# Kernel optimization log

Hardware: AMD Instinct MI355X
Metric: run time of the kernel (lower is better)

The kernel has to match this reference:

```python
import jax, jax.numpy as jnp
import numpy as np

SR = 8                      # search_range
MO = 2 * SR + 1             # max_offset = 17
NC = MO * MO                # 289 cost-volume channels


def _l2_normalize(x, eps=1e-12):
    # torch F.normalize(p=2, dim=1): x / max(||x||_2, eps)
    n = jnp.sqrt(jnp.sum(x * x, axis=1, keepdims=True))
    return x / jnp.maximum(n, eps)


def _conv2d(x, w, b, pad, groups=1):
    out = jax.lax.conv_general_dilated(
        x, w, window_strides=(1, 1), padding=[(pad, pad), (pad, pad)],
        feature_group_count=groups,
        dimension_numbers=('NCHW', 'OIHW', 'NCHW'))
    return out + b[None, :, None, None]


def _cost_volume(x1, x2, sr, norm_both=False):
    x1 = _l2_normalize(x1)
    if norm_both:
        x2 = _l2_normalize(x2)
    bs, c, h, w = x1.shape
    padded = jnp.pad(x2, ((0, 0), (0, 0), (sr, sr), (sr, sr)))
    mo = 2 * sr + 1
    # offsets in (j outer, i inner) order, matching the original double loop
    jj, ii = jnp.meshgrid(jnp.arange(mo), jnp.arange(mo), indexing='ij')
    offs = jnp.stack([jj.reshape(-1), ii.reshape(-1)], axis=-1)  # [mo^2, 2]

    def step(carry, off):
        sl = jax.lax.dynamic_slice(padded, (0, 0, off[0], off[1]), (bs, c, h, w))
        return carry, jnp.mean(x1 * sl, axis=1)  # [bs, h, w]

    _, cv = jax.lax.scan(step, None, offs)       # [mo^2, bs, h, w]
    cv = jnp.transpose(cv, (1, 0, 2, 3))          # [bs, mo^2, h, w]
    return jax.nn.leaky_relu(cv, 0.1)


def setup_inputs() -> dict:
    key = jax.random.key(0)
    ks = jax.random.split(key, 8)
    bs, c, h, w = 4, 256, 64, 64
    scale = 0.05
    return {
        'f1': jax.random.normal(ks[0], (bs, c, h, w), jnp.float32),
        'f2': jax.random.normal(ks[1], (bs, c, h, w), jnp.float32),
        'att_w': jax.random.normal(ks[2], (NC, 1, 7, 7), jnp.float32) * scale,
        'att_b': jax.random.normal(ks[3], (NC,), jnp.float32) * scale,
        'agg1_w': jax.random.normal(ks[4], (NC // 2, NC, 3, 3), jnp.float32) * scale,
        'agg1_b': jax.random.normal(ks[5], (NC // 2,), jnp.float32) * scale,
        'agg2_w': jax.random.normal(ks[6], (49, NC // 2, 3, 3), jnp.float32) * scale,
        'agg2_b': jax.random.normal(ks[7], (49,), jnp.float32) * scale,
    }


def reference(f1, f2, att_w, att_b, agg1_w, agg1_b, agg2_w, agg2_b):
    match_vol = _cost_volume(f1, f2, SR, norm_both=False)          # [bs,289,h,w]
    att = _conv2d(match_vol, att_w, att_b, pad=3, groups=NC)       # depthwise 7x7
    att_vol = match_vol * att
    h1 = jax.nn.relu(_conv2d(att_vol, agg1_w, agg1_b, pad=1))      # Conv(289->144,3)
    out = jax.nn.relu(_conv2d(h1, agg2_w, agg2_b, pad=1))          # Conv(144->49,3)
    return out
```

## Files before the change

### kernel.cpp

```cpp
#include <hip/hip_runtime.h>
#include <hip/hip_bf16.h>

#define BS   4
#define C    256
#define HW   4096
#define NPIX 16384
#define NCH  289
#define MO   17
#define PH   80
#define PW   80
#define C1   144
#define C2   49
#define ASTR 264
#define ICP  320
#define IC3  192
#define CVP  70
#define CVC  320
#define CH64 72

typedef __bf16  bf16x8 __attribute__((ext_vector_type(8)));
typedef float   f32x4  __attribute__((ext_vector_type(4)));
typedef unsigned short us8 __attribute__((ext_vector_type(8)));

__global__ void fused_norm_transpose(const float* __restrict__ f1,
                                     unsigned short* __restrict__ dst) {
    __shared__ float tileT[32 * 257];
    __shared__ float invS[32];
    int blk = blockIdx.x;
    int pblk = blk & 127, b = blk >> 7;
    int p0 = pblk * 32;
    int t = threadIdx.x;
    int tx = t & 31, ty = t >> 5;
    const float* s = f1 + (size_t)b * C * HW;
#pragma unroll
    for (int i = 0; i < 32; ++i) {
        int c = ty + 8 * i;
        tileT[tx * 257 + c] = s[(size_t)c * HW + p0 + tx];
    }
    __syncthreads();
    int lane = t & 63, wave = t >> 6;
    int px = wave * 8 + (lane >> 3);
    int l = lane & 7;
    float ssum = 0.f;
#pragma unroll
    for (int j = 0; j < 32; ++j) {
        float v = tileT[px * 257 + l + 8 * j];
        ssum += v * v;
    }
    ssum += __shfl_xor(ssum, 1);
    ssum += __shfl_xor(ssum, 2);
    ssum += __shfl_xor(ssum, 4);
    if (l == 0) invS[px] = 1.0f / fmaxf(sqrtf(ssum), 1e-12f);
    __syncthreads();
#pragma unroll 4
    for (int p = 0; p < 32; ++p) {
        float v = tileT[p * 257 + t] * invS[p];
        __hip_bfloat16 hb = __float2bfloat16(v);
        dst[((size_t)b * HW + p0 + p) * C + t] = *(unsigned short*)&hb;
    }
}

__global__ void transpose_pad_kernel(const float* __restrict__ src,
                                     unsigned short* __restrict__ dst) {
    __shared__ float tile[32][33];
    int blk = blockIdx.x;
    int pblk = blk & 127;
    int cblk = (blk >> 7) & 7;
    int b    = blk >> 10;
    int tx = threadIdx.x & 31, ty = threadIdx.x >> 5;
    int c0 = cblk * 32, p0 = pblk * 32;
    const float* s = src + (size_t)b * C * HW;
#pragma unroll
    for (int i = 0; i < 4; ++i) {
        int c = c0 + ty + 8 * i;
        tile[ty + 8 * i][tx] = s[(size_t)c * HW + p0 + tx];
    }
    __syncthreads();
#pragma unroll
    for (int i = 0; i < 4; ++i) {
        int p = p0 + ty + 8 * i;
        float v = tile[tx][ty + 8 * i];
        int c = c0 + tx;
        int h = p >> 6, w = p & 63;
        __hip_bfloat16 hb = __float2bfloat16(v);
        dst[(((size_t)b * PH + h + 8) * PW + (w + 8)) * C + c] = *(unsigned short*)&hb;
    }
}

__device__ __forceinline__ void halo_zero_dev(unsigned short* p, int H, int halo,
                                              int Cc, int blk, int t) {
    int W = H;
    int inter = H - 2 * halo;
    int total_pos = H * W - inter * inter;
    int chunks = Cc >> 3;
    size_t tot = (size_t)total_pos * chunks * BS;
    size_t idx = (size_t)blk * 256 + t;
    if (idx >= tot) return;
    int c8 = (int)(idx % chunks);
    size_t r = idx / chunks;
    int pos = (int)(r % total_pos);
    int b = (int)(r / total_pos);
    int h, w;
    int topbot = 2 * halo * W;
    if (pos < halo * W) { h = pos / W; w = pos % W; }
    else if (pos < topbot) { int q = pos - halo * W; h = H - halo + q / W; w = q % W; }
    else {
        int q = pos - topbot;
        int row = q / (2 * halo), off = q % (2 * halo);
        h = halo + row;
        w = (off < halo) ? off : (W - 2 * halo + off);
    }
    us8 z = {0, 0, 0, 0, 0, 0, 0, 0};
    *(us8*)&p[(((size_t)b * H + h) * W + w) * Cc + c8 * 8] = z;
}

__global__ void prep_kernel(unsigned short* __restrict__ x2bf, unsigned short* __restrict__ cvp,
                            unsigned short* __restrict__ avp, unsigned short* __restrict__ h1p,
                            const float* __restrict__ w1, unsigned short* __restrict__ wb1,
                            const float* __restrict__ w2, unsigned short* __restrict__ wb2,
                            const float* __restrict__ att_w, float* __restrict__ wdwp) {
    int blk = blockIdx.x;
    int t = threadIdx.x;
    if (blk < 1152) { halo_zero_dev(x2bf, PH, 8, C, blk, t); return; }
    if (blk < 1655) { halo_zero_dev(cvp, CVP, 3, CVC, blk - 1152, t); return; }
    if (blk < 1818) { halo_zero_dev(avp, 66, 1, ICP, blk - 1655, t); return; }
    if (blk < 1916) { halo_zero_dev(h1p, 66, 1, IC3, blk - 1818, t); return; }
    if (blk < 3536) {
        int idx = (blk - 1916) * 256 + t;
        int tap = idx / (C1 * ICP);
        int r = idx - tap * (C1 * ICP);
        int oc = r / ICP;
        int ic = r - oc * ICP;
        float v = (ic < NCH) ? w1[((size_t)(oc * NCH + ic)) * 9 + tap] : 0.f;
        __hip_bfloat16 hb = __float2bfloat16(v);
        wb1[idx] = *(unsigned short*)&hb;
        return;
    }
    if (blk < 3968) {
        int idx = (blk - 3536) * 256 + t;
        int tap = idx / (64 * IC3);
        int r = idx - tap * (64 * IC3);
        int oc = r / IC3;
        int ic = r - oc * IC3;
        float v = (oc < C2 && ic < C1) ? w2[((size_t)(oc * C1 + ic)) * 9 + tap] : 0.f;
        __hip_bfloat16 hb = __float2bfloat16(v);
        wb2[idx] = *(unsigned short*)&hb;
        return;
    }
    {
        int idx = (blk - 3968) * 256 + t;
        if (idx >= 49 * CVC) return;
        int tap = idx / CVC;
        int ch = idx - tap * CVC;
        wdwp[idx] = (ch < NCH) ? att_w[ch * 49 + tap] : 0.f;
    }
}

__global__ void cv_mfma_kernel(const unsigned short* __restrict__ x1b,
                               const unsigned short* __restrict__ x2b,
                               unsigned short* __restrict__ cvp) {
    __shared__ __align__(16) unsigned short x2s[2][32 * ASTR];
    int i = blockIdx.x;
    int xcd = i & 7;
    int j = i >> 3;
    int hq = xcd * 2 + (j & 1);
    int jj = j >> 1;
    int wseg = jj & 3;
    int b = jj >> 2;
    int h0 = hq * 4;
    int w0 = wseg * 16;
    int t = threadIdx.x;
    int wave = t >> 6, lane = t & 63;
    int lrow = lane & 15, quad = lane >> 4;
    int h = h0 + wave;

    const unsigned short* x1p = x1b + ((size_t)b * HW + h * 64 + w0) * C;
    bf16x8 a[8];
#pragma unroll
    for (int kk = 0; kk < 8; ++kk)
        a[kk] = *(const bf16x8*)&x1p[(size_t)lrow * C + kk * 32 + quad * 8];

    const unsigned short* x2base = x2b + (size_t)b * PH * PW * C;

    {
        const unsigned short* rowp = x2base + ((size_t)h0 * PW + w0) * C;
#pragma unroll
        for (int s = 0; s < 4; ++s) {
            int v = t + s * 256;
            int col = v >> 5, ch8 = v & 31;
            *(us8*)&x2s[0][col * ASTR + ch8 * 8] = *(const us8*)&rowp[(size_t)col * C + ch8 * 8];
        }
    }
    __syncthreads();

    for (int rr = 0; rr < 20; ++rr) {
        us8 pr[4];
        bool dop = (rr + 1 < 20);
        if (dop) {
            const unsigned short* rowp = x2base + ((size_t)(h0 + rr + 1) * PW + w0) * C;
#pragma unroll
            for (int s = 0; s < 4; ++s) {
                int v = t + s * 256;
                int col = v >> 5, ch8 = v & 31;
                pr[s] = *(const us8*)&rowp[(size_t)col * C + ch8 * 8];
            }
        }

        int dj = rr - wave;
        if ((unsigned)dj <= 16u) {
            const unsigned short* xs = x2s[rr & 1];
#pragma unroll
            for (int c = 0; c < 2; ++c) {
                f32x4 acc = {0.f, 0.f, 0.f, 0.f};
#pragma unroll
                for (int kk = 0; kk < 8; ++kk) {
                    bf16x8 bb = *(const bf16x8*)&xs[(c * 16 + lrow) * ASTR + kk * 32 + quad * 8];
                    acc = __builtin_amdgcn_mfma_f32_16x16x32_bf16(a[kk], bb, acc, 0, 0, 0);
                }
#pragma unroll
                for (int r = 0; r < 4; ++r) {
                    int px_l = quad * 4 + r;
                    int di = c * 16 + lrow - px_l;
                    if ((unsigned)di <= 16u) {
                        float v = acc[r] * (1.0f / 256.0f);
                        v = (v > 0.f) ? v : 0.1f * v;
                        __hip_bfloat16 hb = __float2bfloat16(v);
                        cvp[(((size_t)b * CVP + h + 3) * CVP + (w0 + px_l + 3)) * CVC + dj * MO + di] =
                            *(unsigned short*)&hb;
                    }
                }
            }
        }

        if (dop) {
            unsigned short* dst = x2s[(rr + 1) & 1];
#pragma unroll
            for (int s = 0; s < 4; ++s) {
                int v = t + s * 256;
                int col = v >> 5, ch8 = v & 31;
                *(us8*)&dst[col * ASTR + ch8 * 8] = pr[s];
            }
            __syncthreads();
        }
    }
}

__global__ void dw_att_tiled(const unsigned short* __restrict__ cvp,
                             const float* __restrict__ wdwp,
                             const float* __restrict__ att_b, unsigned short* __restrict__ av_pad) {
    __shared__ float actS[14 * 14 * 64];
    __shared__ float wdwS[49 * 64];
    int i = blockIdx.x;
    int ty = i & 7;
    int j = i >> 3;
    int cc = j % 5;
    int rest = j / 5;
    int tx = rest & 7, b = rest >> 3;
    int x0 = tx * 8, y0 = ty * 8;
    int c0 = cc * 64;
    int t = threadIdx.x;

    const unsigned short* cvb = cvp + (((size_t)b * CVP + y0) * CVP + x0) * CVC + c0;
    for (int v = t; v < 14 * 14 * 8; v += 256) {
        int rc = v >> 3, c8v = v & 7;
        int yy = rc / 14, xx = rc - yy * 14;
        bf16x8 raw = *(const bf16x8*)&cvb[((size_t)yy * CVP + xx) * CVC + c8v * 8];
        f32x4 lo, hi;
#pragma unroll
        for (int e = 0; e < 4; ++e) { lo[e] = (float)raw[e]; hi[e] = (float)raw[e + 4]; }
        *(f32x4*)&actS[rc * 64 + c8v * 8] = lo;
        *(f32x4*)&actS[rc * 64 + c8v * 8 + 4] = hi;
    }
    for (int v = t; v < 49 * 64; v += 256) {
        int tap = v >> 6, ch = v & 63;
        wdwS[v] = wdwp[tap * CVC + c0 + ch];
    }
    __syncthreads();

    int ch_l = t & 63, pgrp = t >> 6;
    int ch = c0 + ch_l;
    float bv = (ch < NCH) ? att_b[ch] : 0.f;
    float acc[16];
#pragma unroll
    for (int ii = 0; ii < 16; ++ii) acc[ii] = bv;

    for (int dy = 0; dy < 7; ++dy) {
#pragma unroll
        for (int dx = 0; dx < 7; ++dx) {
            float wv = wdwS[(dy * 7 + dx) * 64 + ch_l];
#pragma unroll
            for (int ii = 0; ii < 16; ++ii) {
                int py = pgrp * 2 + (ii >> 3), px = ii & 7;
                float a = actS[((py + dy) * 14 + (px + dx)) * 64 + ch_l];
                acc[ii] += a * wv;
            }
        }
    }

    if (ch < NCH) {
#pragma unroll
        for (int ii = 0; ii < 16; ++ii) {
            int py = pgrp * 2 + (ii >> 3), px = ii & 7;
            float c0v = actS[((py + 3) * 14 + (px + 3)) * 64 + ch_l];
            __hip_bfloat16 hb = __float2bfloat16(c0v * acc[ii]);
            av_pad[(((size_t)b * 66 + y0 + py + 1) * 66 + (x0 + px + 1)) * ICP + ch] =
                *(unsigned short*)&hb;
        }
    }
}

__global__ void agg1_mfma_kernel(const unsigned short* __restrict__ av_pad,
                                 const unsigned short* __restrict__ wb1,
                                 const float* __restrict__ bias,
                                 unsigned short* __restrict__ h1p) {
    __shared__ __align__(16) unsigned short aS2[2][66 * CH64];
    __shared__ __align__(16) unsigned short bS[2][C1 * CH64];
    int i = blockIdx.x;
    int xcd = i & 7;
    int j = i >> 3;
    int h = xcd * 8 + (j & 7);
    int b = j >> 3;
    int t = threadIdx.x;
    int wave = t >> 6, lane = t & 63;
    int lrow = lane & 15, quad = lane >> 4;
    int ot0 = (wave == 0) ? 0 : (wave * 2 + 1);
    int nt  = (wave == 0) ? 3 : 2;

    f32x4 acc[4][3];
#pragma unroll
    for (int m = 0; m < 4; ++m)
#pragma unroll
        for (int ii = 0; ii < 3; ++ii) acc[m][ii] = (f32x4){0.f, 0.f, 0.f, 0.f};

    const unsigned short* avb = av_pad + (((size_t)b * 66 + h) * 66) * ICP;

    {
        const unsigned short* arow = avb;
#pragma unroll
        for (int s = 0; s < 2; ++s) {
            int v = t + s * 256;
            *(us8*)&aS2[0][(v >> 3) * CH64 + (v & 7) * 8] =
                *(const us8*)&arow[(size_t)(v >> 3) * ICP + (v & 7) * 8];
        }
        if (t < 16) {
            int v = t + 512;
            *(us8*)&aS2[0][(v >> 3) * CH64 + (v & 7) * 8] =
                *(const us8*)&arow[(size_t)(v >> 3) * ICP + (v & 7) * 8];
        }
#pragma unroll
        for (int s = 0; s < 4; ++s) {
            int v = t + s * 256;
            *(us8*)&bS[0][(v >> 3) * CH64 + (v & 7) * 8] =
                *(const us8*)&wb1[(size_t)(v >> 3) * ICP + (v & 7) * 8];
        }
        if (t < 128) {
            int v = t + 1024;
            *(us8*)&bS[0][(v >> 3) * CH64 + (v & 7) * 8] =
                *(const us8*)&wb1[(size_t)(v >> 3) * ICP + (v & 7) * 8];
        }
    }
    __syncthreads();

    for (int k = 0; k < 45; ++k) {
        int rr = k % 15;
        int dx = rr % 3;
        int abuf = (k / 3) & 1, bbuf = k & 1;

        us8 br[5], ar[3];
        int kn = k + 1;
        bool do_b = (kn < 45);
        bool do_a = do_b && (kn % 3 == 0);
        int dyn = kn / 15, rn = kn % 15;
        int ccin = rn / 3, dxn = rn % 3;
        if (do_b) {
            const unsigned short* wt = wb1 + ((size_t)(dyn * 3 + dxn) * C1) * ICP + ccin * 64;
#pragma unroll
            for (int s = 0; s < 4; ++s) {
                int v = t + s * 256;
                br[s] = *(const us8*)&wt[(size_t)(v >> 3) * ICP + (v & 7) * 8];
            }
            if (t < 128) {
                int v = t + 1024;
                br[4] = *(const us8*)&wt[(size_t)(v >> 3) * ICP + (v & 7) * 8];
            }
        }
        if (do_a) {
            const unsigned short* arow = avb + (size_t)dyn * 66 * ICP + ccin * 64;
#pragma unroll
            for (int s = 0; s < 2; ++s) {
                int v = t + s * 256;
                ar[s] = *(const us8*)&arow[(size_t)(v >> 3) * ICP + (v & 7) * 8];
            }
            if (t < 16) {
                int v = t + 512;
                ar[2] = *(const us8*)&arow[(size_t)(v >> 3) * ICP + (v & 7) * 8];
            }
        }

        const unsigned short* aP = aS2[abuf];
        const unsigned short* bP = bS[bbuf];
#pragma unroll
        for (int cc2 = 0; cc2 < 2; ++cc2) {
            bf16x8 bfr[3];
#pragma unroll
            for (int ii = 0; ii < 3; ++ii)
                if (ii < nt)
                    bfr[ii] = *(const bf16x8*)&bP[((ot0 + ii) * 16 + lrow) * CH64 + cc2 * 32 + quad * 8];
#pragma unroll
            for (int m = 0; m < 4; ++m) {
                bf16x8 af = *(const bf16x8*)&aP[(m * 16 + lrow + dx) * CH64 + cc2 * 32 + quad * 8];
#pragma unroll
                for (int ii = 0; ii < 3; ++ii)
                    if (ii < nt)
                        acc[m][ii] = __builtin_amdgcn_mfma_f32_16x16x32_bf16(af, bfr[ii], acc[m][ii], 0, 0, 0);
            }
        }

        if (do_b) {
            unsigned short* dst = bS[bbuf ^ 1];
#pragma unroll
            for (int s = 0; s < 4; ++s) {
                int v = t + s * 256;
                *(us8*)&dst[(v >> 3) * CH64 + (v & 7) * 8] = br[s];
            }
            if (t < 128) {
                int v = t + 1024;
                *(us8*)&dst[(v >> 3) * CH64 + (v & 7) * 8] = br[4];
            }
        }
        if (do_a) {
            unsigned short* dst = aS2[abuf ^ 1];
#pragma unroll
            for (int s = 0; s < 2; ++s) {
                int v = t + s * 256;
                *(us8*)&dst[(v >> 3) * CH64 + (v & 7) * 8] = ar[s];
            }
            if (t < 16) {
                int v = t + 512;
                *(us8*)&dst[(v >> 3) * CH64 + (v & 7) * 8] = ar[2];
            }
        }
        if (do_b) __syncthreads();
    }

    size_t rowbase = ((size_t)b * 66 + h + 1) * 66;
#pragma unroll
    for (int m = 0; m < 4; ++m)
#pragma unroll
        for (int ii = 0; ii < 3; ++ii)
            if (ii < nt) {
                int oc = (ot0 + ii) * 16 + lrow;
                float bv = bias[oc];
#pragma unroll
                for (int r = 0; r < 4; ++r) {
                    int w = m * 16 + quad * 4 + r;
                    float val = fmaxf(acc[m][ii][r] + bv, 0.f);
                    __hip_bfloat16 hb = __float2bfloat16(val);
                    h1p[(rowbase + (w + 1)) * IC3 + oc] = *(unsigned short*)&hb;
                }
            }
}

__global__ void agg2_mfma_kernel(const unsigned short* __restrict__ h1p,
                                 const unsigned short* __restrict__ wb2,
                                 const float* __restrict__ bias, float* __restrict__ out) {
    __shared__ __align__(16) unsigned short aS2[2][66 * CH64];
    __shared__ __align__(16) unsigned short bS2[2][64 * CH64];
    int i = blockIdx.x;
    int xcd = i & 7;
    int j = i >> 3;
    int h = xcd * 8 + (j & 7);
    int b = j >> 3;
    int t = threadIdx.x;
    int wave = t >> 6, lane = t & 63;
    int lrow = lane & 15, quad = lane >> 4;
    int pt = wave;

    f32x4 acc[4];
#pragma unroll
    for (int ot = 0; ot < 4; ++ot) acc[ot] = (f32x4){0.f, 0.f, 0.f, 0.f};

    const unsigned short* h1b = h1p + (((size_t)b * 66 + h) * 66) * IC3;

    {
#pragma unroll
        for (int s = 0; s < 2; ++s) {
            int v = t + s * 256;
            *(us8*)&aS2[0][(v >> 3) * CH64 + (v & 7) * 8] =
                *(const us8*)&h1b[(size_t)(v >> 3) * IC3 + (v & 7) * 8];
        }
        if (t < 16) {
            int v = t + 512;
            *(us8*)&aS2[0][(v >> 3) * CH64 + (v & 7) * 8] =
                *(const us8*)&h1b[(size_t)(v >> 3) * IC3 + (v & 7) * 8];
        }
#pragma unroll
        for (int s = 0; s < 2; ++s) {
            int v = t + s * 256;
            *(us8*)&bS2[0][(v >> 3) * CH64 + (v & 7) * 8] =
                *(const us8*)&wb2[(size_t)(v >> 3) * IC3 + (v & 7) * 8];
        }
    }
    __syncthreads();

    for (int k = 0; k < 27; ++k) {
        int rem = k % 9;
        int dx = rem % 3;
        int abuf = (k / 3) & 1, bbuf = k & 1;

        us8 br[2], ar[3];
        int kn = k + 1;
        bool do_b = (kn < 27);
        bool do_a = do_b && (kn % 3 == 0);
        int dyn = kn / 9, rn = kn % 9;
        int ccn = rn / 3, dxn = rn % 3;
        if (do_b) {
            const unsigned short* wt = wb2 + ((size_t)(dyn * 3 + dxn) * 64) * IC3 + ccn * 64;
#pragma unroll
            for (int s = 0; s < 2; ++s) {
                int v = t + s * 256;
                br[s] = *(const us8*)&wt[(size_t)(v >> 3) * IC3 + (v & 7) * 8];
            }
        }
        if (do_a) {
            const unsigned short* arow = h1b + (size_t)dyn * 66 * IC3 + ccn * 64;
#pragma unroll
            for (int s = 0; s < 2; ++s) {
                int v = t + s * 256;
                ar[s] = *(const us8*)&arow[(size_t)(v >> 3) * IC3 + (v & 7) * 8];
            }
            if (t < 16) {
                int v = t + 512;
                ar[2] = *(const us8*)&arow[(size_t)(v >> 3) * IC3 + (v & 7) * 8];
            }
        }

        const unsigned short* aP = aS2[abuf];
        const unsigned short* bP = bS2[bbuf];
#pragma unroll
        for (int cc2 = 0; cc2 < 2; ++cc2) {
            bf16x8 af = *(const bf16x8*)&aP[(pt * 16 + lrow + dx) * CH64 + cc2 * 32 + quad * 8];
#pragma unroll
            for (int ot = 0; ot < 4; ++ot) {
                bf16x8 bfr = *(const bf16x8*)&bP[(ot * 16 + lrow) * CH64 + cc2 * 32 + quad * 8];
                acc[ot] = __builtin_amdgcn_mfma_f32_16x16x32_bf16(af, bfr, acc[ot], 0, 0, 0);
            }
        }

        if (do_b) {
            unsigned short* dst = bS2[bbuf ^ 1];
#pragma unroll
            for (int s = 0; s < 2; ++s) {
                int v = t + s * 256;
                *(us8*)&dst[(v >> 3) * CH64 + (v & 7) * 8] = br[s];
            }
        }
        if (do_a) {
            unsigned short* dst = aS2[abuf ^ 1];
#pragma unroll
            for (int s = 0; s < 2; ++s) {
                int v = t + s * 256;
                *(us8*)&dst[(v >> 3) * CH64 + (v & 7) * 8] = ar[s];
            }
            if (t < 16) {
                int v = t + 512;
                *(us8*)&dst[(v >> 3) * CH64 + (v & 7) * 8] = ar[2];
            }
        }
        if (do_b) __syncthreads();
    }

#pragma unroll
    for (int ot = 0; ot < 4; ++ot) {
        int o = ot * 16 + lrow;
        if (o < C2) {
            float bv = bias[o];
#pragma unroll
            for (int r = 0; r < 4; ++r) {
                int w = pt * 16 + quad * 4 + r;
                out[((size_t)b * C2 + o) * HW + h * 64 + w] = fmaxf(acc[ot][r] + bv, 0.f);
            }
        }
    }
}

extern "C" void kernel_launch(void* const* d_in, const int* in_sizes, int n_in,
                              void* d_out, int out_size, void* d_ws, size_t ws_size,
                              hipStream_t stream) {
    const float* f1    = (const float*)d_in[0];
    const float* f2    = (const float*)d_in[1];
    const float* att_w = (const float*)d_in[2];
    const float* att_b = (const float*)d_in[3];
    const float* w1    = (const float*)d_in[4];
    const float* b1    = (const float*)d_in[5];
    const float* w2    = (const float*)d_in[6];
    const float* b2    = (const float*)d_in[7];
    float* out = (float*)d_out;

    char* wsb = (char*)d_ws;
    size_t off = 0;
    float* wdwp = (float*)(wsb + off); off += (size_t)49 * CVC * 4;
    off = (off + 15) & ~(size_t)15;
    unsigned short* x1bf = (unsigned short*)(wsb + off); off += (size_t)NPIX * C * 2;
    unsigned short* x2bf = (unsigned short*)(wsb + off); off += (size_t)BS * PH * PW * C * 2;
    unsigned short* cvp  = (unsigned short*)(wsb + off); off += (size_t)BS * CVP * CVP * CVC * 2;
    unsigned short* avp  = (unsigned short*)(wsb + off); off += (size_t)BS * 66 * 66 * ICP * 2;
    unsigned short* wb1  = (unsigned short*)(wsb + off); off += (size_t)9 * C1 * ICP * 2;
    unsigned short* h1p  = (unsigned short*)(wsb + off); off += (size_t)BS * 66 * 66 * IC3 * 2;
    unsigned short* wb2  = (unsigned short*)(wsb + off); off += (size_t)9 * 64 * IC3 * 2;
    if (ws_size < off) return;

    prep_kernel<<<4030, 256, 0, stream>>>(x2bf, cvp, avp, h1p, w1, wb1, w2, wb2, att_w, wdwp);
    fused_norm_transpose<<<512, 256, 0, stream>>>(f1, x1bf);
    transpose_pad_kernel<<<4096, 256, 0, stream>>>(f2, x2bf);

    cv_mfma_kernel<<<256, 256, 0, stream>>>(x1bf, x2bf, cvp);
    dw_att_tiled<<<1280, 256, 0, stream>>>(cvp, wdwp, att_b, avp);
    agg1_mfma_kernel<<<256, 256, 0, stream>>>(avp, wb1, b1, h1p);
    agg2_mfma_kernel<<<256, 256, 0, stream>>>(h1p, wb2, b2, out);
}
```

Measured before the change: 195.5 us.

## Merge prep kernels, split cost-volume work across more blocks, register-tile depthwise conv

Folds the prep, normalize-transpose and pad-transpose kernels into one setup launch, which removes two kernel launches and their gaps. The cost-volume kernel now runs 512 blocks covering 2 rows each, with every wave doing one 16-column MFMA tile instead of two. That gives more parallelism and less per-wave work, but each block re-streams more overlapping x2 rows (19 per 2 rows instead of 20 per 4). The depthwise 7x7 loop loads one row of 14 activations and 7 weights into registers so each LDS value is reused across taps.

```diff
diff --git a/kernel.cpp b/kernel.cpp
--- a/kernel.cpp
+++ b/kernel.cpp
@@ -21,71 +21,6 @@
 typedef __bf16  bf16x8 __attribute__((ext_vector_type(8)));
 typedef float   f32x4  __attribute__((ext_vector_type(4)));
 typedef unsigned short us8 __attribute__((ext_vector_type(8)));
-
-__global__ void fused_norm_transpose(const float* __restrict__ f1,
-                                     unsigned short* __restrict__ dst) {
-    __shared__ float tileT[32 * 257];
-    __shared__ float invS[32];
-    int blk = blockIdx.x;
-    int pblk = blk & 127, b = blk >> 7;
-    int p0 = pblk * 32;
-    int t = threadIdx.x;
-    int tx = t & 31, ty = t >> 5;
-    const float* s = f1 + (size_t)b * C * HW;
-#pragma unroll
-    for (int i = 0; i < 32; ++i) {
-        int c = ty + 8 * i;
-        tileT[tx * 257 + c] = s[(size_t)c * HW + p0 + tx];
-    }
-    __syncthreads();
-    int lane = t & 63, wave = t >> 6;
-    int px = wave * 8 + (lane >> 3);
-    int l = lane & 7;
-    float ssum = 0.f;
-#pragma unroll
-    for (int j = 0; j < 32; ++j) {
-        float v = tileT[px * 257 + l + 8 * j];
-        ssum += v * v;
-    }
-    ssum += __shfl_xor(ssum, 1);
-    ssum += __shfl_xor(ssum, 2);
-    ssum += __shfl_xor(ssum, 4);
-    if (l == 0) invS[px] = 1.0f / fmaxf(sqrtf(ssum), 1e-12f);
-    __syncthreads();
-#pragma unroll 4
-    for (int p = 0; p < 32; ++p) {
-        float v = tileT[p * 257 + t] * invS[p];
-        __hip_bfloat16 hb = __float2bfloat16(v);
-        dst[((size_t)b * HW + p0 + p) * C + t] = *(unsigned short*)&hb;
-    }
-}
-
-__global__ void transpose_pad_kernel(const float* __restrict__ src,
-                                     unsigned short* __restrict__ dst) {
-    __shared__ float tile[32][33];
-    int blk = blockIdx.x;
-    int pblk = blk & 127;
-    int cblk = (blk >> 7) & 7;
-    int b    = blk >> 10;
-    int tx = threadIdx.x & 31, ty = threadIdx.x >> 5;
-    int c0 = cblk * 32, p0 = pblk * 32;
-    const float* s = src + (size_t)b * C * HW;
-#pragma unroll
-    for (int i = 0; i < 4; ++i) {
-        int c = c0 + ty + 8 * i;
-        tile[ty + 8 * i][tx] = s[(size_t)c * HW + p0 + tx];
-    }
-    __syncthreads();
-#pragma unroll
-    for (int i = 0; i < 4; ++i) {
-        int p = p0 + ty + 8 * i;
-        float v = tile[tx][ty + 8 * i];
-        int c = c0 + tx;
-        int h = p >> 6, w = p & 63;
-        __hip_bfloat16 hb = __float2bfloat16(v);
-        dst[(((size_t)b * PH + h + 8) * PW + (w + 8)) * C + c] = *(unsigned short*)&hb;
-    }
-}
 
 __device__ __forceinline__ void halo_zero_dev(unsigned short* p, int H, int halo,
                                               int Cc, int blk, int t) {
@@ -114,65 +49,135 @@
     *(us8*)&p[(((size_t)b * H + h) * W + w) * Cc + c8 * 8] = z;
 }
 
-__global__ void prep_kernel(unsigned short* __restrict__ x2bf, unsigned short* __restrict__ cvp,
-                            unsigned short* __restrict__ avp, unsigned short* __restrict__ h1p,
-                            const float* __restrict__ w1, unsigned short* __restrict__ wb1,
-                            const float* __restrict__ w2, unsigned short* __restrict__ wb2,
-                            const float* __restrict__ att_w, float* __restrict__ wdwp) {
+__global__ void setup_kernel(unsigned short* __restrict__ x2bf, unsigned short* __restrict__ cvp,
+                             unsigned short* __restrict__ avp, unsigned short* __restrict__ h1p,
+                             const float* __restrict__ w1, unsigned short* __restrict__ wb1,
+                             const float* __restrict__ w2, unsigned short* __restrict__ wb2,
+                             const float* __restrict__ att_w, float* __restrict__ wdwp,
+                             const float* __restrict__ f1, unsigned short* __restrict__ x1bf,
+                             const float* __restrict__ f2) {
+    __shared__ float shmem[32 * 257 + 32];
     int blk = blockIdx.x;
     int t = threadIdx.x;
-    if (blk < 1152) { halo_zero_dev(x2bf, PH, 8, C, blk, t); return; }
-    if (blk < 1655) { halo_zero_dev(cvp, CVP, 3, CVC, blk - 1152, t); return; }
-    if (blk < 1818) { halo_zero_dev(avp, 66, 1, ICP, blk - 1655, t); return; }
-    if (blk < 1916) { halo_zero_dev(h1p, 66, 1, IC3, blk - 1818, t); return; }
-    if (blk < 3536) {
-        int idx = (blk - 1916) * 256 + t;
-        int tap = idx / (C1 * ICP);
-        int r = idx - tap * (C1 * ICP);
-        int oc = r / ICP;
-        int ic = r - oc * ICP;
-        float v = (ic < NCH) ? w1[((size_t)(oc * NCH + ic)) * 9 + tap] : 0.f;
-        __hip_bfloat16 hb = __float2bfloat16(v);
-        wb1[idx] = *(unsigned short*)&hb;
+    if (blk < 4030) {
+        if (blk < 1152) { halo_zero_dev(x2bf, PH, 8, C, blk, t); return; }
+        if (blk < 1655) { halo_zero_dev(cvp, CVP, 3, CVC, blk - 1152, t); return; }
+        if (blk < 1818) { halo_zero_dev(avp, 66, 1, ICP, blk - 1655, t); return; }
+        if (blk < 1916) { halo_zero_dev(h1p, 66, 1, IC3, blk - 1818, t); return; }
+        if (blk < 3536) {
+            int idx = (blk - 1916) * 256 + t;
+            int tap = idx / (C1 * ICP);
+            int r = idx - tap * (C1 * ICP);
+            int oc = r / ICP;
+            int ic = r - oc * ICP;
+            float v = (ic < NCH) ? w1[((size_t)(oc * NCH + ic)) * 9 + tap] : 0.f;
+            __hip_bfloat16 hb = __float2bfloat16(v);
+            wb1[idx] = *(unsigned short*)&hb;
+            return;
+        }
+        if (blk < 3968) {
+            int idx = (blk - 3536) * 256 + t;
+            int tap = idx / (64 * IC3);
+            int r = idx - tap * (64 * IC3);
+            int oc = r / IC3;
+            int ic = r - oc * IC3;
+            float v = (oc < C2 && ic < C1) ? w2[((size_t)(oc * C1 + ic)) * 9 + tap] : 0.f;
+            __hip_bfloat16 hb = __float2bfloat16(v);
+            wb2[idx] = *(unsigned short*)&hb;
+            return;
+        }
+        {
+            int idx = (blk - 3968) * 256 + t;
+            if (idx >= 49 * CVC) return;
+            int tap = idx / CVC;
+            int ch = idx - tap * CVC;
+            wdwp[idx] = (ch < NCH) ? att_w[ch * 49 + tap] : 0.f;
+        }
         return;
     }
-    if (blk < 3968) {
-        int idx = (blk - 3536) * 256 + t;
-        int tap = idx / (64 * IC3);
-        int r = idx - tap * (64 * IC3);
-        int oc = r / IC3;
-        int ic = r - oc * IC3;
-        float v = (oc < C2 && ic < C1) ? w2[((size_t)(oc * C1 + ic)) * 9 + tap] : 0.f;
-        __hip_bfloat16 hb = __float2bfloat16(v);
-        wb2[idx] = *(unsigned short*)&hb;
+    if (blk < 4542) {
+        float* tileT = shmem;
+        float* invS = shmem + 32 * 257;
+        int bb = blk - 4030;
+        int pblk = bb & 127, b = bb >> 7;
+        int p0 = pblk * 32;
+        int tx = t & 31, ty = t >> 5;
+        const float* s = f1 + (size_t)b * C * HW;
+#pragma unroll
+        for (int i = 0; i < 32; ++i) {
+            int c = ty + 8 * i;
+            tileT[tx * 257 + c] = s[(size_t)c * HW + p0 + tx];
+        }
+        __syncthreads();
+        int lane = t & 63, wave = t >> 6;
+        int px = wave * 8 + (lane >> 3);
+        int l = lane & 7;
+        float ssum = 0.f;
+#pragma unroll
+        for (int j = 0; j < 32; ++j) {
+            float v = tileT[px * 257 + l + 8 * j];
+            ssum += v * v;
+        }
+        ssum += __shfl_xor(ssum, 1);
+        ssum += __shfl_xor(ssum, 2);
+        ssum += __shfl_xor(ssum, 4);
+        if (l == 0) invS[px] = 1.0f / fmaxf(sqrtf(ssum), 1e-12f);
+        __syncthreads();
+#pragma unroll 4
+        for (int p = 0; p < 32; ++p) {
+            float v = tileT[p * 257 + t] * invS[p];
+            __hip_bfloat16 hb = __float2bfloat16(v);
+            x1bf[((size_t)b * HW + p0 + p) * C + t] = *(unsigned short*)&hb;
+        }
         return;
     }
     {
-        int idx = (blk - 3968) * 256 + t;
-        if (idx >= 49 * CVC) return;
-        int tap = idx / CVC;
-        int ch = idx - tap * CVC;
-        wdwp[idx] = (ch < NCH) ? att_w[ch * 49 + tap] : 0.f;
+        float* tile = shmem;
+        int bb = blk - 4542;
+        int pblk = bb & 127;
+        int cblk = (bb >> 7) & 7;
+        int b    = bb >> 10;
+        int tx = t & 31, ty = t >> 5;
+        int c0 = cblk * 32, p0 = pblk * 32;
+        const float* s = f2 + (size_t)b * C * HW;
+#pragma unroll
+        for (int i = 0; i < 4; ++i) {
+            int c = c0 + ty + 8 * i;
+            tile[(ty + 8 * i) * 33 + tx] = s[(size_t)c * HW + p0 + tx];
+        }
+        __syncthreads();
+#pragma unroll
+        for (int i = 0; i < 4; ++i) {
+            int p = p0 + ty + 8 * i;
+            float v = tile[tx * 33 + ty + 8 * i];
+            int c = c0 + tx;
+            int h = p >> 6, w = p & 63;
+            __hip_bfloat16 hb = __float2bfloat16(v);
+            x2bf[(((size_t)b * PH + h + 8) * PW + (w + 8)) * C + c] = *(unsigned short*)&hb;
+        }
     }
 }
 
-__global__ void cv_mfma_kernel(const unsigned short* __restrict__ x1b,
-                               const unsigned short* __restrict__ x2b,
-                               unsigned short* __restrict__ cvp) {
+__global__ __launch_bounds__(256, 2)
+void cv_mfma_kernel(const unsigned short* __restrict__ x1b,
+                    const unsigned short* __restrict__ x2b,
+                    unsigned short* __restrict__ cvp) {
     __shared__ __align__(16) unsigned short x2s[2][32 * ASTR];
     int i = blockIdx.x;
     int xcd = i & 7;
     int j = i >> 3;
-    int hq = xcd * 2 + (j & 1);
-    int jj = j >> 1;
+    int hp = xcd * 4 + (j & 3);
+    int jj = j >> 2;
     int wseg = jj & 3;
     int b = jj >> 2;
-    int h0 = hq * 4;
+    int h0 = hp * 2;
     int w0 = wseg * 16;
     int t = threadIdx.x;
     int wave = t >> 6, lane = t & 63;
     int lrow = lane & 15, quad = lane >> 4;
-    int h = h0 + wave;
+    int row_w = wave >> 1, ct = wave & 1;
+    int h = h0 + row_w;
+    int col_l = ct * 16 + lrow;
 
     const unsigned short* x1p = x1b + ((size_t)b * HW + h * 64 + w0) * C;
     bf16x8 a[8];
@@ -193,9 +198,9 @@
     }
     __syncthreads();
 
-    for (int rr = 0; rr < 20; ++rr) {
+    for (int rr = 0; rr < 19; ++rr) {
         us8 pr[4];
-        bool dop = (rr + 1 < 20);
+        bool dop = (rr + 1 < 19);
         if (dop) {
             const unsigned short* rowp = x2base + ((size_t)(h0 + rr + 1) * PW + w0) * C;
 #pragma unroll
@@ -206,28 +211,25 @@
             }
         }
 
-        int dj = rr - wave;
+        int dj = rr - row_w;
         if ((unsigned)dj <= 16u) {
             const unsigned short* xs = x2s[rr & 1];
-#pragma unroll
-            for (int c = 0; c < 2; ++c) {
-                f32x4 acc = {0.f, 0.f, 0.f, 0.f};
-#pragma unroll
-                for (int kk = 0; kk < 8; ++kk) {
-                    bf16x8 bb = *(const bf16x8*)&xs[(c * 16 + lrow) * ASTR + kk * 32 + quad * 8];
-                    acc = __builtin_amdgcn_mfma_f32_16x16x32_bf16(a[kk], bb, acc, 0, 0, 0);
-                }
-#pragma unroll
-                for (int r = 0; r < 4; ++r) {
-                    int px_l = quad * 4 + r;
-                    int di = c * 16 + lrow - px_l;
-                    if ((unsigned)di <= 16u) {
-                        float v = acc[r] * (1.0f / 256.0f);
-                        v = (v > 0.f) ? v : 0.1f * v;
-                        __hip_bfloat16 hb = __float2bfloat16(v);
-                        cvp[(((size_t)b * CVP + h + 3) * CVP + (w0 + px_l + 3)) * CVC + dj * MO + di] =
-                            *(unsigned short*)&hb;
-                    }
+            f32x4 acc = {0.f, 0.f, 0.f, 0.f};
+#pragma unroll
+            for (int kk = 0; kk < 8; ++kk) {
+                bf16x8 bb = *(const bf16x8*)&xs[col_l * ASTR + kk * 32 + quad * 8];
+                acc = __builtin_amdgcn_mfma_f32_16x16x32_bf16(a[kk], bb, acc, 0, 0, 0);
+            }
+#pragma unroll
+            for (int r = 0; r < 4; ++r) {
+                int px_l = quad * 4 + r;
+                int di = col_l - px_l;
+                if ((unsigned)di <= 16u) {
+                    float v = acc[r] * (1.0f / 256.0f);
+                    v = (v > 0.f) ? v : 0.1f * v;
+                    __hip_bfloat16 hb = __float2bfloat16(v);
+                    cvp[(((size_t)b * CVP + h + 3) * CVP + (w0 + px_l + 3)) * CVC + dj * MO + di] =
+                        *(unsigned short*)&hb;
                 }
             }
         }
@@ -285,15 +287,22 @@
     for (int ii = 0; ii < 16; ++ii) acc[ii] = bv;
 
     for (int dy = 0; dy < 7; ++dy) {
-#pragma unroll
-        for (int dx = 0; dx < 7; ++dx) {
-            float wv = wdwS[(dy * 7 + dx) * 64 + ch_l];
-#pragma unroll
-            for (int ii = 0; ii < 16; ++ii) {
-                int py = pgrp * 2 + (ii >> 3), px = ii & 7;
-                float a = actS[((py + dy) * 14 + (px + dx)) * 64 + ch_l];
-                acc[ii] += a * wv;
-            }
+        float wreg[7];
+#pragma unroll
+        for (int dx = 0; dx < 7; ++dx)
+            wreg[dx] = wdwS[(dy * 7 + dx) * 64 + ch_l];
+#pragma unroll
+        for (int py2 = 0; py2 < 2; ++py2) {
+            int row = pgrp * 2 + py2 + dy;
+            float rowv[14];
+#pragma unroll
+            for (int xx = 0; xx < 14; ++xx)
+                rowv[xx] = actS[(row * 14 + xx) * 64 + ch_l];
+#pragma unroll
+            for (int dx = 0; dx < 7; ++dx)
+#pragma unroll
+                for (int px = 0; px < 8; ++px)
+                    acc[py2 * 8 + px] += rowv[px + dx] * wreg[dx];
         }
     }
 
@@ -610,11 +619,9 @@
     unsigned short* wb2  = (unsigned short*)(wsb + off); off += (size_t)9 * 64 * IC3 * 2;
     if (ws_size < off) return;
 
-    prep_kernel<<<4030, 256, 0, stream>>>(x2bf, cvp, avp, h1p, w1, wb1, w2, wb2, att_w, wdwp);
-    fused_norm_transpose<<<512, 256, 0, stream>>>(f1, x1bf);
-    transpose_pad_kernel<<<4096, 256, 0, stream>>>(f2, x2bf);
-
-    cv_mfma_kernel<<<256, 256, 0, stream>>>(x1bf, x2bf, cvp);
+    setup_kernel<<<8638, 256, 0, stream>>>(x2bf, cvp, avp, h1p, w1, wb1, w2, wb2,
+                                           att_w, wdwp, f1, x1bf, f2);
+    cv_mfma_kernel<<<512, 256, 0, stream>>>(x1bf, x2bf, cvp);
     dw_att_tiled<<<1280, 256, 0, stream>>>(cvp, wdwp, att_b, avp);
     agg1_mfma_kernel<<<256, 256, 0, stream>>>(avp, wb1, b1, h1p);
     agg2_mfma_kernel<<<256, 256, 0, stream>>>(h1p, wb2, b2, out);
```

Measured after the change: 187.0 us. 1.05x faster.
